# Kernel tuning notes

Hardware: AMD Instinct MI355X
Metric: run time of the kernel (lower is better)

Reference implementation:

```python
import jax, jax.numpy as jnp
import numpy as np

B, D, H, W = 4, 64, 64, 64
S = 64          # number of attention segments
N = 8192        # query pixels
K = 4           # n_refs
HID = 256
D9 = D * 9      # feat_unfold 3x3
IN_DIM = D9 + 2 + 2  # +rel_coord +rel_cell


def setup_inputs() -> dict:
    key = jax.random.key(0)
    ks = jax.random.split(key, 10)
    feat = jax.random.normal(ks[0], (B, D, H, W), jnp.float32)
    attn_sftmx = jax.nn.softmax(jax.random.normal(ks[1], (B, H * W, S), jnp.float32), axis=2)
    coord = jax.random.uniform(ks[2], (B, N, 2), jnp.float32) * 2.0 - 1.0  # [-1,1]
    cell = jnp.full((B, N, 2), 2.0 / 256.0, jnp.float32)  # HR cell size for 256x256 output
    def lin(k, fi, fo):
        return jax.random.normal(k, (fi, fo), jnp.float32) / np.sqrt(fi).astype(np.float32)
    w0 = lin(ks[3], IN_DIM, HID); b0 = jnp.zeros((HID,), jnp.float32)
    w1 = lin(ks[4], HID, HID);    b1 = jnp.zeros((HID,), jnp.float32)
    w2 = lin(ks[5], HID, HID);    b2 = jnp.zeros((HID,), jnp.float32)
    w3 = lin(ks[6], HID, HID);    b3 = jnp.zeros((HID,), jnp.float32)
    w4 = lin(ks[7], HID, 3);      b4 = jnp.zeros((3,), jnp.float32)
    return dict(feat=feat, attn_sftmx=attn_sftmx, coord=coord, cell=cell,
                w0=w0, b0=b0, w1=w1, b1=b1, w2=w2, b2=b2, w3=w3, b3=b3, w4=w4, b4=b4)


def _imnet(x, w0, b0, w1, b1, w2, b2, w3, b3, w4, b4):
    h = jax.nn.relu(x @ w0 + b0)
    h = jax.nn.relu(h @ w1 + b1)
    h = jax.nn.relu(h @ w2 + b2)
    h = jax.nn.relu(h @ w3 + b3)
    return h @ w4 + b4


def reference(feat, attn_sftmx, coord, cell, w0, b0, w1, b1, w2, b2, w3, b3, w4, b4):
    Bn, Dc, h, w = feat.shape
    Nq = coord.shape[1]
    hw = h * w
    # ---- feat_unfold: F.unfold(feat, 3, padding=1) -> (B, D*9, h, w), channel order c*9 + ki*3 + kj
    pad = jnp.pad(feat, ((0, 0), (0, 0), (1, 1), (1, 1)))
    patches = jnp.stack([pad[:, :, ki:ki + h, kj:kj + w]
                         for ki in range(3) for kj in range(3)], axis=2)  # (B,D,9,h,w)
    d9 = Dc * 9
    feat_rows = patches.reshape(Bn, d9, h, w).transpose(0, 2, 3, 1).reshape(Bn, hw, d9)  # (B,hw,D9)
    scale_hw = jnp.array([h, w], jnp.float32)
    rel_cell = cell * scale_hw  # (B,N,2)

    # ================= attention ensemble =================
    pc = (coord + 1.0) / 2.0 * scale_hw
    pc = jnp.clip(pc.astype(jnp.int32), 0, hw - 1)
    pc1d = pc[..., 0] * h + pc[..., 1]  # (B,N)
    segm_idx_whole = jnp.argmax(attn_sftmx, axis=2)  # (B,hw)
    segm_idx = jnp.take_along_axis(segm_idx_whole, pc1d, axis=1)  # (B,N)
    attn_t = attn_sftmx.transpose(0, 2, 1)  # (B,S,hw)
    prob_map = jnp.take_along_axis(attn_t, segm_idx[:, :, None], axis=1)  # (B,N,hw)
    ref_probs, ref_coords = jax.lax.top_k(prob_map, K)  # (B,N,K)
    # Faithful to original: ref_coords (values in [0,hw)) index the FLATTENED (B*hw, D9)
    # feature table, i.e. all batches gather batch-0 rows (source-code behavior).
    ref_feats = feat_rows.reshape(Bn * hw, d9)[ref_coords]  # (B,N,K,D9)
    rrc = ref_coords - pc1d[..., None]  # (B,N,K) int
    rel0 = jnp.floor_divide(rrc, h).astype(jnp.float32) / h
    rel1 = jnp.mod(rrc, h).astype(jnp.float32) / w
    rel = jnp.stack([rel0, rel1], axis=-1)  # (B,N,K,2)
    rc_b = jnp.broadcast_to(rel_cell[:, :, None, :], (Bn, Nq, K, 2))
    inp_attn = jnp.concatenate([ref_feats, rel, rc_b], axis=-1)  # (B,N,K,IN)
    pred_attn = _imnet(inp_attn.reshape(-1, inp_attn.shape[-1]),
                       w0, b0, w1, b1, w2, b2, w3, b3, w4, b4).reshape(Bn, Nq, K, -1)
    wprob = ref_probs / jnp.sum(ref_probs, axis=-1, keepdims=True)
    ret_attn = jnp.sum(pred_attn * wprob[..., None], axis=2)  # (B,N,3)

    # ================= local ensemble =================
    rx, ry = 1.0 / h, 1.0 / w  # 2/h/2, 2/w/2
    eps = 1e-6
    offs = jnp.array([[-1., -1.], [-1., 1.], [1., -1.], [1., 1.]], jnp.float32) \
           * jnp.array([rx, ry], jnp.float32) + eps  # (4,2)
    c = jnp.clip(coord[None] + offs[:, None, None, :], -1 + 1e-6, 1 - 1e-6)  # (4,B,N,2)
    # grid_sample nearest, align_corners=False (grid flipped -> c[...,0] is height)
    iy = jnp.clip(jnp.rint(((c[..., 0] + 1.0) * h - 1.0) / 2.0), 0, h - 1).astype(jnp.int32)
    ix = jnp.clip(jnp.rint(((c[..., 1] + 1.0) * w - 1.0) / 2.0), 0, w - 1).astype(jnp.int32)
    flat = iy * w + ix  # (4,B,N)
    bidx = jnp.arange(Bn)[None, :, None]
    q_feat = feat_rows[bidx, flat]  # (4,B,N,D9)
    qc0 = -1.0 + (2.0 * iy.astype(jnp.float32) + 1.0) / h  # make_coord centers
    qc1 = -1.0 + (2.0 * ix.astype(jnp.float32) + 1.0) / w
    rel_coord = jnp.stack([(coord[None, ..., 0] - qc0) * h,
                           (coord[None, ..., 1] - qc1) * w], axis=-1)  # (4,B,N,2)
    rc_l = jnp.broadcast_to(rel_cell[None], (4, Bn, Nq, 2))
    inp_loc = jnp.concatenate([q_feat, rel_coord, rc_l], axis=-1)  # (4,B,N,IN)
    pred_loc = _imnet(inp_loc.reshape(-1, inp_loc.shape[-1]),
                      w0, b0, w1, b1, w2, b2, w3, b3, w4, b4).reshape(4, Bn, Nq, -1)
    area = jnp.abs(rel_coord[..., 0] * rel_coord[..., 1]) + 1e-9  # (4,B,N)
    tot = jnp.sum(area, axis=0)
    wts = area[::-1] / tot[None]  # area swap 0<->3, 1<->2 == reverse
    ret_local = jnp.sum(pred_loc * wts[..., None], axis=0)  # (B,N,3)

    total = float(K + 4)
    return ret_attn * (K / total) + ret_local * (4.0 / total)
```

## Files before the change

kernel.cpp:

```cpp
#include <hip/hip_runtime.h>
#include <hip/hip_bf16.h>
#include <math.h>
#include <stdint.h>

#define B_ 4
#define D_ 64
#define H_ 64
#define W_ 64
#define S_ 64
#define N_ 8192
#define K_ 4
#define HID_ 256
#define HW_ 4096
#define NQ_ (B_*N_)
#define ROWS_ (NQ_*8)

typedef _Float16 h8   __attribute__((ext_vector_type(8)));
typedef _Float16 h4   __attribute__((ext_vector_type(4)));
typedef float    f32x4 __attribute__((ext_vector_type(4)));

__global__ void fused_prep_kernel(const float* __restrict__ feat,
                                  const float* __restrict__ attn,
                                  const float* __restrict__ w0,
                                  const float* __restrict__ w1,
                                  const float* __restrict__ w2,
                                  const float* __restrict__ w3,
                                  const float* __restrict__ w4,
                                  _Float16* __restrict__ featT,
                                  _Float16* __restrict__ w0F,
                                  _Float16* __restrict__ wF123,
                                  float* __restrict__ w4T,
                                  float* __restrict__ w0tail,
                                  int* __restrict__ segm,
                                  float* __restrict__ pv,
                                  int* __restrict__ pi)
{
  __shared__ float t[64][65];
  int blk = blockIdx.x;
  int tid = threadIdx.x;

  if (blk < 256) {
    int b = blk >> 6, y = blk & 63;
    for (int p = 0; p < 16; ++p) {
      int c = p * 4 + (tid >> 6), x = tid & 63;
      t[c][x] = feat[(((size_t)b * 64 + c) << 12) + (y << 6) + x];
    }
    __syncthreads();
    for (int p = 0; p < 16; ++p) {
      int x = p * 4 + (tid >> 6), c = tid & 63;
      featT[((((size_t)b * 64 + y) * 64 + x) << 6) + c] = (_Float16)t[c][x];
    }
    return;
  }
  blk -= 256;
  if (blk < 1351) {
    int i = blk * 256 + tid;
    if (i < 147456) {
      int g = i / 36864, rem = i - g * 36864;
      int ks = rem >> 11, rem2 = rem & 2047;
      int cb = rem2 >> 9, e = rem2 & 511;
      int lane = e >> 3, j = e & 7;
      int n = g * 64 + cb * 16 + (lane & 15);
      int k = ks * 32 + (lane >> 4) * 8 + j;
      int kk = k >> 6, cc = k & 63;
      w0F[i] = (_Float16)w0[(cc * 9 + kk) * 256 + n];
      return;
    }
    i -= 147456;
    if (i < 196608) {
      int l = i >> 16, rem = i & 65535;
      int g = rem >> 14, rem2 = rem & 16383;
      int ks = rem2 >> 11, rem3 = rem2 & 2047;
      int cb = rem3 >> 9, e = rem3 & 511;
      int lane = e >> 3, j = e & 7;
      int n = g * 64 + cb * 16 + (lane & 15);
      int k = ks * 32 + (lane >> 4) * 8 + j;
      const float* w = (l == 0) ? w1 : (l == 1) ? w2 : w3;
      wF123[i] = (_Float16)w[k * 256 + n];
      return;
    }
    i -= 196608;
    if (i < 768) { int j = i / 256, c = i - j * 256; w4T[i] = w4[c * 3 + j]; return; }
    i -= 768;
    if (i < 1024) { int j = i >> 8, n = i & 255; w0tail[i] = w0[(576 + j) * 256 + n]; }
    return;
  }
  blk -= 1351;
  {
    int b = blk >> 6, chunk = blk & 63;
    int j0 = chunk * 64;
    for (int idx = tid; idx < 4096; idx += 256) {
      int r = idx >> 6, c = idx & 63;
      t[r][c] = attn[((size_t)(b * 4096 + j0 + r)) * 64 + c];
    }
    __syncthreads();
    if (tid >= 64 && tid < 128) {
      int r = tid - 64;
      float best = t[r][0]; int bi = 0;
      for (int s = 1; s < 64; ++s) { float v = t[r][s]; if (v > best) { best = v; bi = s; } }
      segm[b * 4096 + j0 + r] = bi;
    } else if (tid < 64) {
      int s = tid;
      float tv[4] = { -INFINITY, -INFINITY, -INFINITY, -INFINITY };
      int   ti[4] = { 0x7fffffff, 0x7fffffff, 0x7fffffff, 0x7fffffff };
      for (int r = 0; r < 64; ++r) {
        float v = t[r][s];
        if (v > tv[3]) {
          tv[3] = v; ti[3] = j0 + r;
          #pragma unroll
          for (int x = 3; x > 0; --x) {
            if (tv[x] > tv[x-1] || (tv[x] == tv[x-1] && ti[x] < ti[x-1])) {
              float fv = tv[x]; tv[x] = tv[x-1]; tv[x-1] = fv;
              int   fi = ti[x]; ti[x] = ti[x-1]; ti[x-1] = fi;
            }
          }
        }
      }
      size_t base = (((size_t)(b * 64 + s)) * 64 + chunk) * 4;
      #pragma unroll
      for (int k = 0; k < 4; ++k) { pv[base + k] = tv[k]; pi[base + k] = ti[k]; }
    }
  }
}

__global__ void meta_kernel(const float* __restrict__ coord, const float* __restrict__ cell,
                            const int* __restrict__ segm,
                            const float* __restrict__ pv, const int* __restrict__ pi,
                            int* __restrict__ msrc, float4* __restrict__ mt,
                            float* __restrict__ mwgt)
{
  __shared__ int   refcL[64][4];
  __shared__ float wprobL[64][4];
  int tid = threadIdx.x;
  int bb = blockIdx.x >> 5;
  if (tid < 64) {
    int s = tid;
    float tv[4] = { -INFINITY, -INFINITY, -INFINITY, -INFINITY };
    int   ti[4] = { 0x7fffffff, 0x7fffffff, 0x7fffffff, 0x7fffffff };
    size_t base = ((size_t)(bb * 64 + s)) * 256;
    for (int c = 0; c < 256; ++c) {
      float v = pv[base + c]; int ix = pi[base + c];
      if (v > tv[3] || (v == tv[3] && ix < ti[3])) {
        tv[3] = v; ti[3] = ix;
        #pragma unroll
        for (int x = 3; x > 0; --x) {
          if (tv[x] > tv[x-1] || (tv[x] == tv[x-1] && ti[x] < ti[x-1])) {
            float fv = tv[x]; tv[x] = tv[x-1]; tv[x-1] = fv;
            int   fi = ti[x]; ti[x] = ti[x-1]; ti[x-1] = fi;
          }
        }
      }
    }
    float ssum = tv[0] + tv[1] + tv[2] + tv[3];
    #pragma unroll
    for (int k = 0; k < 4; ++k) { refcL[s][k] = ti[k]; wprobL[s][k] = tv[k] / ssum; }
  }
  __syncthreads();

  int q = blockIdx.x * 256 + tid;
  int b = q >> 13;
  float c0 = coord[2*q], c1 = coord[2*q + 1];
  float rc0 = cell[2*q] * 64.0f, rc1 = cell[2*q + 1] * 64.0f;

  float pf0 = (c0 + 1.0f) / 2.0f * 64.0f;
  float pf1 = (c1 + 1.0f) / 2.0f * 64.0f;
  int pc0 = (int)pf0, pc1 = (int)pf1;
  pc0 = min(max(pc0, 0), 4095); pc1 = min(max(pc1, 0), 4095);
  int pc1d = pc0 * 64 + pc1;
  int sg = segm[b * 4096 + min(pc1d, 4095)];
  #pragma unroll
  for (int k = 0; k < 4; ++k) {
    int rc = refcL[sg][k];
    int rrc = rc - pc1d;
    float rel0 = (float)(rrc >> 6) * 0.015625f;
    float rel1 = (float)(rrc & 63) * 0.015625f;
    int r = q * 8 + k;
    msrc[r] = rc;
    mt[r] = make_float4(rel0, rel1, rc0, rc1);
    mwgt[r] = 0.5f * wprobL[sg][k];
  }

  const float sg0[4] = { -1.f, -1.f, 1.f, 1.f };
  const float sg1[4] = { -1.f,  1.f, -1.f, 1.f };
  float area[4], rr0[4], rr1[4]; int srcs[4];
  #pragma unroll
  for (int tt = 0; tt < 4; ++tt) {
    float o0 = sg0[tt] * 0.015625f + 1e-6f;
    float o1 = sg1[tt] * 0.015625f + 1e-6f;
    float cc0 = fminf(fmaxf(c0 + o0, -1.0f + 1e-6f), 1.0f - 1e-6f);
    float cc1 = fminf(fmaxf(c1 + o1, -1.0f + 1e-6f), 1.0f - 1e-6f);
    float vy = ((cc0 + 1.0f) * 64.0f - 1.0f) / 2.0f;
    float vx = ((cc1 + 1.0f) * 64.0f - 1.0f) / 2.0f;
    float fy = fminf(fmaxf(rintf(vy), 0.0f), 63.0f);
    float fx = fminf(fmaxf(rintf(vx), 0.0f), 63.0f);
    int iy = (int)fy, ix = (int)fx;
    srcs[tt] = b * 4096 + iy * 64 + ix;
    float qc0 = -1.0f + (2.0f * (float)iy + 1.0f) / 64.0f;
    float qc1 = -1.0f + (2.0f * (float)ix + 1.0f) / 64.0f;
    float r0 = (c0 - qc0) * 64.0f;
    float r1 = (c1 - qc1) * 64.0f;
    rr0[tt] = r0; rr1[tt] = r1;
    area[tt] = fabsf(r0 * r1) + 1e-9f;
  }
  float tot = area[0] + area[1] + area[2] + area[3];
  #pragma unroll
  for (int tt = 0; tt < 4; ++tt) {
    int r = q * 8 + 4 + tt;
    msrc[r] = srcs[tt];
    mt[r] = make_float4(rr0[tt], rr1[tt], rc0, rc1);
    mwgt[r] = 0.5f * area[3 - tt] / tot;
  }
}

__launch_bounds__(256, 2)
__global__ void p0_kernel(const _Float16* __restrict__ featT,
                          const _Float16* __restrict__ w0F,
                          _Float16* __restrict__ P0h)
{
  int blk = blockIdx.x;
  int b = blk >> 7, y = (blk >> 1) & 63, hr = blk & 1;
  int tid = threadIdx.x;
  int wave = tid >> 6, lane = tid & 63, quad = lane >> 4, l16 = lane & 15;

  f32x4 acc[2][4];
  #pragma unroll
  for (int i = 0; i < 2; i++)
    #pragma unroll
    for (int j = 0; j < 4; j++) { f32x4 z = {0.f,0.f,0.f,0.f}; acc[i][j] = z; }
  h8 zero8 = {0,0,0,0,0,0,0,0};

  #pragma unroll
  for (int ks = 0; ks < 18; ++ks) {
    int k0 = ks * 32 + quad * 8;
    int kk = k0 >> 6, cc = k0 & 63;
    int di = kk / 3 - 1, dj = kk - (kk / 3) * 3 - 1;
    int yy = y + di;
    h8 afr[2];
    #pragma unroll
    for (int rb = 0; rb < 2; rb++) {
      int xx = hr * 32 + rb * 16 + l16 + dj;
      if ((unsigned)yy < 64u && (unsigned)xx < 64u)
        afr[rb] = *(const h8*)(featT + ((((size_t)b * 64 + yy) * 64 + xx) << 6) + cc);
      else
        afr[rb] = zero8;
    }
    h8 bfr[4];
    #pragma unroll
    for (int cb = 0; cb < 4; cb++)
      bfr[cb] = *(const h8*)(w0F + ((((size_t)wave * 18 + ks) * 4 + cb) << 9) + lane * 8);
    #pragma unroll
    for (int rb = 0; rb < 2; rb++)
      #pragma unroll
      for (int cb = 0; cb < 4; cb++)
        acc[rb][cb] = __builtin_amdgcn_mfma_f32_16x16x32_f16(afr[rb], bfr[cb], acc[rb][cb], 0, 0, 0);
  }
  int pixbase = b * 4096 + y * 64 + hr * 32;
  #pragma unroll
  for (int rb = 0; rb < 2; rb++)
    #pragma unroll
    for (int cb = 0; cb < 4; cb++)
      #pragma unroll
      for (int i = 0; i < 4; i++) {
        int m = rb * 16 + quad * 4 + i;
        int n = wave * 64 + cb * 16 + l16;
        P0h[((size_t)(pixbase + m) << 8) + n] = (_Float16)acc[rb][cb][i];
      }
}

__launch_bounds__(256, 2)
__global__ void trunk_kernel(const _Float16* __restrict__ P0h,
                             const int* __restrict__ msrc,
                             const float4* __restrict__ mt,
                             const float* __restrict__ mwgt,
                             const float* __restrict__ w0tail,
                             const float* __restrict__ b0,
                             const _Float16* __restrict__ wF123,
                             const float* __restrict__ b1,
                             const float* __restrict__ b2,
                             const float* __restrict__ b3,
                             const float* __restrict__ w4T,
                             const float* __restrict__ b4,
                             float* __restrict__ out)
{
  __shared__ _Float16 hS[128][264];
  __shared__ float mwL[128];
  __shared__ float swL[16];
  __shared__ float partB[16][3][4];

  int tid = threadIdx.x;
  int rowbase = blockIdx.x * 128;
  int wv = tid >> 6;

  if (tid < 128) mwL[tid] = mwgt[rowbase + tid];

  {
    int cg = tid & 63;
    float4 wt0 = ((const float4*)w0tail)[cg];
    float4 wt1 = ((const float4*)w0tail)[64 + cg];
    float4 wt2 = ((const float4*)w0tail)[128 + cg];
    float4 wt3 = ((const float4*)w0tail)[192 + cg];
    float4 bb  = ((const float4*)b0)[cg];
    #pragma unroll 1
    for (int g = 0; g < 4; ++g) {
      int srcs[8]; float4 ts[8];
      #pragma unroll
      for (int i = 0; i < 8; ++i) {
        int r = rowbase + g * 32 + i * 4 + wv;
        srcs[i] = msrc[r];
        ts[i] = mt[r];
      }
      #pragma unroll
      for (int i = 0; i < 8; ++i) {
        int rr = g * 32 + i * 4 + wv;
        float4 t = ts[i];
        h4 pvv = *(const h4*)(P0h + ((size_t)srcs[i] << 8) + cg * 4);
        h4 v;
        v[0] = (_Float16)fmaxf((float)pvv[0] + t.x*wt0.x + t.y*wt1.x + t.z*wt2.x + t.w*wt3.x + bb.x, 0.0f);
        v[1] = (_Float16)fmaxf((float)pvv[1] + t.x*wt0.y + t.y*wt1.y + t.z*wt2.y + t.w*wt3.y + bb.y, 0.0f);
        v[2] = (_Float16)fmaxf((float)pvv[2] + t.x*wt0.z + t.y*wt1.z + t.z*wt2.z + t.w*wt3.z + bb.z, 0.0f);
        v[3] = (_Float16)fmaxf((float)pvv[3] + t.x*wt0.w + t.y*wt1.w + t.z*wt2.w + t.w*wt3.w + bb.w, 0.0f);
        *(h4*)(&hS[rr][cg * 4]) = v;
      }
    }
  }
  __syncthreads();

  int wave = tid >> 6, lane = tid & 63, quad = lane >> 4, l16 = lane & 15;

  #pragma unroll 1
  for (int l = 0; l < 3; ++l) {
    const _Float16* wL = wF123 + (((size_t)l * 4 + wave) << 14);
    const float* bia = (l == 0) ? b1 : (l == 1) ? b2 : b3;
    f32x4 acc[8][4];
    #pragma unroll
    for (int i = 0; i < 8; i++)
      #pragma unroll
      for (int j = 0; j < 4; j++) { f32x4 z = {0.f,0.f,0.f,0.f}; acc[i][j] = z; }

    h8 bP[2][4];
    #pragma unroll
    for (int cb = 0; cb < 4; cb++) {
      bP[0][cb] = *(const h8*)(wL + (((size_t)0 * 4 + cb) << 9) + lane * 8);
      bP[1][cb] = *(const h8*)(wL + (((size_t)1 * 4 + cb) << 9) + lane * 8);
    }

    #pragma unroll
    for (int ks = 0; ks < 8; ++ks) {
      int cur = ks & 1;
      int k0 = ks * 32 + quad * 8;
      h8 afr[8];
      #pragma unroll
      for (int rb = 0; rb < 8; rb++)
        afr[rb] = *(const h8*)(&hS[rb * 16 + l16][k0]);
      #pragma unroll
      for (int rb = 0; rb < 8; rb++)
        #pragma unroll
        for (int cb = 0; cb < 4; cb++)
          acc[rb][cb] = __builtin_amdgcn_mfma_f32_16x16x32_f16(afr[rb], bP[cur][cb], acc[rb][cb], 0, 0, 0);
      if (ks + 2 < 8) {
        #pragma unroll
        for (int cb = 0; cb < 4; cb++)
          bP[cur][cb] = *(const h8*)(wL + (((size_t)(ks + 2) * 4 + cb) << 9) + lane * 8);
      }
    }
    __syncthreads();
    #pragma unroll
    for (int rb = 0; rb < 8; rb++)
      #pragma unroll
      for (int cb = 0; cb < 4; cb++) {
        int n = wave * 64 + cb * 16 + l16;
        float bv = bia[n];
        #pragma unroll
        for (int i = 0; i < 4; i++) {
          int m = rb * 16 + quad * 4 + i;
          hS[m][n] = (_Float16)fmaxf(acc[rb][cb][i] + bv, 0.0f);
        }
      }
    __syncthreads();
  }

  {
    if (tid < 16) {
      float sw = 0.0f;
      #pragma unroll
      for (int j = 0; j < 8; ++j) sw += mwL[tid * 8 + j];
      swL[tid] = sw;
    }
    int c = tid;
    float accq[16];
    #pragma unroll
    for (int u = 0; u < 16; ++u) accq[u] = 0.0f;
    #pragma unroll
    for (int row = 0; row < 128; ++row) {
      float w = mwL[row];
      accq[row >> 3] += w * (float)hS[row][c];
    }
    __syncthreads();
    float* hsF = (float*)&hS[0][0];
    #pragma unroll
    for (int q = 0; q < 16; ++q) hsF[q * 256 + c] = accq[q];
  }
  __syncthreads();
  if (tid < 192) {
    int q = tid / 12, r = tid % 12, j = r >> 2, part = r & 3;
    const float* hsF = (const float*)&hS[0][0];
    const float* hp = hsF + q * 256 + part * 64;
    const float* wp = w4T + j * 256 + part * 64;
    int u0 = tid & 63;
    float s = 0.0f;
    #pragma unroll
    for (int u = 0; u < 64; ++u) {
      int uu = (u0 + u) & 63;
      s += hp[uu] * wp[uu];
    }
    partB[q][j][part] = s;
  }
  __syncthreads();
  if (tid < 48) {
    int q = tid / 3, j = tid % 3;
    float o = partB[q][j][0] + partB[q][j][1] + partB[q][j][2] + partB[q][j][3]
            + b4[j] * swL[q];
    out[(size_t)(blockIdx.x * 16 + q) * 3 + j] = o;
  }
}

extern "C" void kernel_launch(void* const* d_in, const int* in_sizes, int n_in,
                              void* d_out, int out_size, void* d_ws, size_t ws_size,
                              hipStream_t stream)
{
  const float* feat  = (const float*)d_in[0];
  const float* attn  = (const float*)d_in[1];
  const float* coord = (const float*)d_in[2];
  const float* cell  = (const float*)d_in[3];
  const float* w0 = (const float*)d_in[4];
  const float* b0 = (const float*)d_in[5];
  const float* w1 = (const float*)d_in[6];
  const float* b1 = (const float*)d_in[7];
  const float* w2 = (const float*)d_in[8];
  const float* b2 = (const float*)d_in[9];
  const float* w3 = (const float*)d_in[10];
  const float* b3 = (const float*)d_in[11];
  const float* w4 = (const float*)d_in[12];
  const float* b4 = (const float*)d_in[13];
  float* out = (float*)d_out;

  char* ws = (char*)d_ws;
  size_t off = 0;
  auto alloc = [&](size_t bytes) -> char* {
    char* p = ws + off;
    off += (bytes + 255) & ~(size_t)255;
    return p;
  };
  _Float16* featT = (_Float16*)alloc((size_t)B_ * H_ * W_ * D_ * 2);
  _Float16* w0F   = (_Float16*)alloc((size_t)147456 * 2);
  _Float16* wF123 = (_Float16*)alloc((size_t)196608 * 2);
  float*  w4T   = (float*)alloc((size_t)3 * 256 * 4);
  float*  w0tl  = (float*)alloc((size_t)4 * 256 * 4);
  int*    segm  = (int*)alloc((size_t)B_ * HW_ * 4);
  float*  pv    = (float*)alloc((size_t)B_ * S_ * 64 * 4 * 4);
  int*    pi    = (int*)alloc((size_t)B_ * S_ * 64 * 4 * 4);
  _Float16* P0h = (_Float16*)alloc((size_t)B_ * HW_ * 256 * 2);
  int*    msrc  = (int*)alloc((size_t)ROWS_ * 4);
  float4* mtb   = (float4*)alloc((size_t)ROWS_ * 16);
  float*  mwgt  = (float*)alloc((size_t)ROWS_ * 4);
  (void)in_sizes; (void)n_in; (void)out_size; (void)ws_size;

  fused_prep_kernel<<<1863, 256, 0, stream>>>(feat, attn, w0, w1, w2, w3, w4,
                                              featT, w0F, wF123, w4T, w0tl,
                                              segm, pv, pi);
  meta_kernel<<<128, 256, 0, stream>>>(coord, cell, segm, pv, pi, msrc, mtb, mwgt);
  p0_kernel<<<512, 256, 0, stream>>>(featT, w0F, P0h);
  trunk_kernel<<<2048, 256, 0, stream>>>(P0h, msrc, mtb, mwgt, w0tl, b0, wF123,
                                         b1, b2, b3, w4T, b4, out);
}
```

Before: 291.4 us.

## Move per-segment top-4 merge into extra p0 block, vectorize trunk reduction

The segment top-4 merge, which meta_kernel used to recompute redundantly in every block, now runs once in a single extra block (block 512) of p0_kernel and writes refc and wprob to global memory. meta_kernel becomes a purely per-query kernel that reads those arrays. This removes duplicated serial work, at the cost of one block doing a long serial merge inside p0. The trunk epilogue's weighted row reduction is also rewritten so each thread reads 16 consecutive channels of its query's 8 rows with vector loads and stores. The rotated index in the final dot product is dropped, which may bring back LDS bank conflicts.

```diff
diff --git a/kernel.cpp b/kernel.cpp
--- a/kernel.cpp
+++ b/kernel.cpp
@@ -123,21 +123,19 @@
   }
 }
 
-__global__ void meta_kernel(const float* __restrict__ coord, const float* __restrict__ cell,
-                            const int* __restrict__ segm,
-                            const float* __restrict__ pv, const int* __restrict__ pi,
-                            int* __restrict__ msrc, float4* __restrict__ mt,
-                            float* __restrict__ mwgt)
+__launch_bounds__(256, 2)
+__global__ void p0_kernel(const _Float16* __restrict__ featT,
+                          const _Float16* __restrict__ w0F,
+                          const float* __restrict__ pv, const int* __restrict__ pi,
+                          _Float16* __restrict__ P0h,
+                          int* __restrict__ refc, float* __restrict__ wprob)
 {
-  __shared__ int   refcL[64][4];
-  __shared__ float wprobL[64][4];
+  int blk = blockIdx.x;
   int tid = threadIdx.x;
-  int bb = blockIdx.x >> 5;
-  if (tid < 64) {
-    int s = tid;
+  if (blk == 512) {
     float tv[4] = { -INFINITY, -INFINITY, -INFINITY, -INFINITY };
     int   ti[4] = { 0x7fffffff, 0x7fffffff, 0x7fffffff, 0x7fffffff };
-    size_t base = ((size_t)(bb * 64 + s)) * 256;
+    size_t base = (size_t)tid * 256;
     for (int c = 0; c < 256; ++c) {
       float v = pv[base + c]; int ix = pi[base + c];
       if (v > tv[3] || (v == tv[3] && ix < ti[3])) {
@@ -153,11 +151,66 @@
     }
     float ssum = tv[0] + tv[1] + tv[2] + tv[3];
     #pragma unroll
-    for (int k = 0; k < 4; ++k) { refcL[s][k] = ti[k]; wprobL[s][k] = tv[k] / ssum; }
-  }
-  __syncthreads();
-
-  int q = blockIdx.x * 256 + tid;
+    for (int k = 0; k < 4; ++k) { refc[tid*4 + k] = ti[k]; wprob[tid*4 + k] = tv[k] / ssum; }
+    return;
+  }
+
+  int b = blk >> 7, y = (blk >> 1) & 63, hr = blk & 1;
+  int wave = tid >> 6, lane = tid & 63, quad = lane >> 4, l16 = lane & 15;
+
+  f32x4 acc[2][4];
+  #pragma unroll
+  for (int i = 0; i < 2; i++)
+    #pragma unroll
+    for (int j = 0; j < 4; j++) { f32x4 z = {0.f,0.f,0.f,0.f}; acc[i][j] = z; }
+  h8 zero8 = {0,0,0,0,0,0,0,0};
+
+  #pragma unroll
+  for (int ks = 0; ks < 18; ++ks) {
+    int k0 = ks * 32 + quad * 8;
+    int kk = k0 >> 6, cc = k0 & 63;
+    int di = kk / 3 - 1, dj = kk - (kk / 3) * 3 - 1;
+    int yy = y + di;
+    h8 afr[2];
+    #pragma unroll
+    for (int rb = 0; rb < 2; rb++) {
+      int xx = hr * 32 + rb * 16 + l16 + dj;
+      if ((unsigned)yy < 64u && (unsigned)xx < 64u)
+        afr[rb] = *(const h8*)(featT + ((((size_t)b * 64 + yy) * 64 + xx) << 6) + cc);
+      else
+        afr[rb] = zero8;
+    }
+    h8 bfr[4];
+    #pragma unroll
+    for (int cb = 0; cb < 4; cb++)
+      bfr[cb] = *(const h8*)(w0F + ((((size_t)wave * 18 + ks) * 4 + cb) << 9) + lane * 8);
+    #pragma unroll
+    for (int rb = 0; rb < 2; rb++)
+      #pragma unroll
+      for (int cb = 0; cb < 4; cb++)
+        acc[rb][cb] = __builtin_amdgcn_mfma_f32_16x16x32_f16(afr[rb], bfr[cb], acc[rb][cb], 0, 0, 0);
+  }
+  int pixbase = b * 4096 + y * 64 + hr * 32;
+  #pragma unroll
+  for (int rb = 0; rb < 2; rb++)
+    #pragma unroll
+    for (int cb = 0; cb < 4; cb++)
+      #pragma unroll
+      for (int i = 0; i < 4; i++) {
+        int m = rb * 16 + quad * 4 + i;
+        int n = wave * 64 + cb * 16 + l16;
+        P0h[((size_t)(pixbase + m) << 8) + n] = (_Float16)acc[rb][cb][i];
+      }
+}
+
+__global__ void meta_kernel(const float* __restrict__ coord, const float* __restrict__ cell,
+                            const int* __restrict__ segm, const int* __restrict__ refc,
+                            const float* __restrict__ wprob,
+                            int* __restrict__ msrc, float4* __restrict__ mt,
+                            float* __restrict__ mwgt)
+{
+  int q = blockIdx.x * 256 + threadIdx.x;
+  if (q >= NQ_) return;
   int b = q >> 13;
   float c0 = coord[2*q], c1 = coord[2*q + 1];
   float rc0 = cell[2*q] * 64.0f, rc1 = cell[2*q + 1] * 64.0f;
@@ -168,25 +221,26 @@
   pc0 = min(max(pc0, 0), 4095); pc1 = min(max(pc1, 0), 4095);
   int pc1d = pc0 * 64 + pc1;
   int sg = segm[b * 4096 + min(pc1d, 4095)];
+  int base = (b * 64 + sg) * 4;
   #pragma unroll
   for (int k = 0; k < 4; ++k) {
-    int rc = refcL[sg][k];
+    int rc = refc[base + k];
     int rrc = rc - pc1d;
     float rel0 = (float)(rrc >> 6) * 0.015625f;
     float rel1 = (float)(rrc & 63) * 0.015625f;
     int r = q * 8 + k;
     msrc[r] = rc;
     mt[r] = make_float4(rel0, rel1, rc0, rc1);
-    mwgt[r] = 0.5f * wprobL[sg][k];
+    mwgt[r] = 0.5f * wprob[base + k];
   }
 
   const float sg0[4] = { -1.f, -1.f, 1.f, 1.f };
   const float sg1[4] = { -1.f,  1.f, -1.f, 1.f };
   float area[4], rr0[4], rr1[4]; int srcs[4];
   #pragma unroll
-  for (int tt = 0; tt < 4; ++tt) {
-    float o0 = sg0[tt] * 0.015625f + 1e-6f;
-    float o1 = sg1[tt] * 0.015625f + 1e-6f;
+  for (int t = 0; t < 4; ++t) {
+    float o0 = sg0[t] * 0.015625f + 1e-6f;
+    float o1 = sg1[t] * 0.015625f + 1e-6f;
     float cc0 = fminf(fmaxf(c0 + o0, -1.0f + 1e-6f), 1.0f - 1e-6f);
     float cc1 = fminf(fmaxf(c1 + o1, -1.0f + 1e-6f), 1.0f - 1e-6f);
     float vy = ((cc0 + 1.0f) * 64.0f - 1.0f) / 2.0f;
@@ -194,77 +248,22 @@
     float fy = fminf(fmaxf(rintf(vy), 0.0f), 63.0f);
     float fx = fminf(fmaxf(rintf(vx), 0.0f), 63.0f);
     int iy = (int)fy, ix = (int)fx;
-    srcs[tt] = b * 4096 + iy * 64 + ix;
+    srcs[t] = b * 4096 + iy * 64 + ix;
     float qc0 = -1.0f + (2.0f * (float)iy + 1.0f) / 64.0f;
     float qc1 = -1.0f + (2.0f * (float)ix + 1.0f) / 64.0f;
     float r0 = (c0 - qc0) * 64.0f;
     float r1 = (c1 - qc1) * 64.0f;
-    rr0[tt] = r0; rr1[tt] = r1;
-    area[tt] = fabsf(r0 * r1) + 1e-9f;
+    rr0[t] = r0; rr1[t] = r1;
+    area[t] = fabsf(r0 * r1) + 1e-9f;
   }
   float tot = area[0] + area[1] + area[2] + area[3];
   #pragma unroll
-  for (int tt = 0; tt < 4; ++tt) {
-    int r = q * 8 + 4 + tt;
-    msrc[r] = srcs[tt];
-    mt[r] = make_float4(rr0[tt], rr1[tt], rc0, rc1);
-    mwgt[r] = 0.5f * area[3 - tt] / tot;
-  }
-}
-
-__launch_bounds__(256, 2)
-__global__ void p0_kernel(const _Float16* __restrict__ featT,
-                          const _Float16* __restrict__ w0F,
-                          _Float16* __restrict__ P0h)
-{
-  int blk = blockIdx.x;
-  int b = blk >> 7, y = (blk >> 1) & 63, hr = blk & 1;
-  int tid = threadIdx.x;
-  int wave = tid >> 6, lane = tid & 63, quad = lane >> 4, l16 = lane & 15;
-
-  f32x4 acc[2][4];
-  #pragma unroll
-  for (int i = 0; i < 2; i++)
-    #pragma unroll
-    for (int j = 0; j < 4; j++) { f32x4 z = {0.f,0.f,0.f,0.f}; acc[i][j] = z; }
-  h8 zero8 = {0,0,0,0,0,0,0,0};
-
-  #pragma unroll
-  for (int ks = 0; ks < 18; ++ks) {
-    int k0 = ks * 32 + quad * 8;
-    int kk = k0 >> 6, cc = k0 & 63;
-    int di = kk / 3 - 1, dj = kk - (kk / 3) * 3 - 1;
-    int yy = y + di;
-    h8 afr[2];
-    #pragma unroll
-    for (int rb = 0; rb < 2; rb++) {
-      int xx = hr * 32 + rb * 16 + l16 + dj;
-      if ((unsigned)yy < 64u && (unsigned)xx < 64u)
-        afr[rb] = *(const h8*)(featT + ((((size_t)b * 64 + yy) * 64 + xx) << 6) + cc);
-      else
-        afr[rb] = zero8;
-    }
-    h8 bfr[4];
-    #pragma unroll
-    for (int cb = 0; cb < 4; cb++)
-      bfr[cb] = *(const h8*)(w0F + ((((size_t)wave * 18 + ks) * 4 + cb) << 9) + lane * 8);
-    #pragma unroll
-    for (int rb = 0; rb < 2; rb++)
-      #pragma unroll
-      for (int cb = 0; cb < 4; cb++)
-        acc[rb][cb] = __builtin_amdgcn_mfma_f32_16x16x32_f16(afr[rb], bfr[cb], acc[rb][cb], 0, 0, 0);
-  }
-  int pixbase = b * 4096 + y * 64 + hr * 32;
-  #pragma unroll
-  for (int rb = 0; rb < 2; rb++)
-    #pragma unroll
-    for (int cb = 0; cb < 4; cb++)
-      #pragma unroll
-      for (int i = 0; i < 4; i++) {
-        int m = rb * 16 + quad * 4 + i;
-        int n = wave * 64 + cb * 16 + l16;
-        P0h[((size_t)(pixbase + m) << 8) + n] = (_Float16)acc[rb][cb][i];
-      }
+  for (int t = 0; t < 4; ++t) {
+    int r = q * 8 + 4 + t;
+    msrc[r] = srcs[t];
+    mt[r] = make_float4(rr0[t], rr1[t], rc0, rc1);
+    mwgt[r] = 0.5f * area[3 - t] / tot;
+  }
 }
 
 __launch_bounds__(256, 2)
@@ -380,25 +379,31 @@
   }
 
   {
-    if (tid < 16) {
-      float sw = 0.0f;
-      #pragma unroll
-      for (int j = 0; j < 8; ++j) sw += mwL[tid * 8 + j];
-      swL[tid] = sw;
-    }
-    int c = tid;
+    int q = tid >> 4, cpart = tid & 15;
     float accq[16];
     #pragma unroll
     for (int u = 0; u < 16; ++u) accq[u] = 0.0f;
-    #pragma unroll
-    for (int row = 0; row < 128; ++row) {
+    float sw = 0.0f;
+    #pragma unroll
+    for (int j = 0; j < 8; ++j) {
+      int row = q * 8 + j;
       float w = mwL[row];
-      accq[row >> 3] += w * (float)hS[row][c];
+      sw += w;
+      h8 a = *(const h8*)(&hS[row][cpart * 16]);
+      h8 bq = *(const h8*)(&hS[row][cpart * 16 + 8]);
+      #pragma unroll
+      for (int u = 0; u < 8; ++u) {
+        accq[u]     += w * (float)a[u];
+        accq[8 + u] += w * (float)bq[u];
+      }
     }
     __syncthreads();
     float* hsF = (float*)&hS[0][0];
     #pragma unroll
-    for (int q = 0; q < 16; ++q) hsF[q * 256 + c] = accq[q];
+    for (int u = 0; u < 16; u += 4)
+      *(f32x4*)(hsF + q * 256 + cpart * 16 + u) =
+        f32x4{accq[u], accq[u+1], accq[u+2], accq[u+3]};
+    if (cpart == 0) swL[q] = sw;
   }
   __syncthreads();
   if (tid < 192) {
@@ -406,13 +411,9 @@
     const float* hsF = (const float*)&hS[0][0];
     const float* hp = hsF + q * 256 + part * 64;
     const float* wp = w4T + j * 256 + part * 64;
-    int u0 = tid & 63;
     float s = 0.0f;
     #pragma unroll
-    for (int u = 0; u < 64; ++u) {
-      int uu = (u0 + u) & 63;
-      s += hp[uu] * wp[uu];
-    }
+    for (int u = 0; u < 64; ++u) s += hp[u] * wp[u];
     partB[q][j][part] = s;
   }
   __syncthreads();
@@ -459,6 +460,8 @@
   int*    segm  = (int*)alloc((size_t)B_ * HW_ * 4);
   float*  pv    = (float*)alloc((size_t)B_ * S_ * 64 * 4 * 4);
   int*    pi    = (int*)alloc((size_t)B_ * S_ * 64 * 4 * 4);
+  int*    refc  = (int*)alloc((size_t)B_ * S_ * K_ * 4);
+  float*  wprob = (float*)alloc((size_t)B_ * S_ * K_ * 4);
   _Float16* P0h = (_Float16*)alloc((size_t)B_ * HW_ * 256 * 2);
   int*    msrc  = (int*)alloc((size_t)ROWS_ * 4);
   float4* mtb   = (float4*)alloc((size_t)ROWS_ * 16);
@@ -468,8 +471,8 @@
   fused_prep_kernel<<<1863, 256, 0, stream>>>(feat, attn, w0, w1, w2, w3, w4,
                                               featT, w0F, wF123, w4T, w0tl,
                                               segm, pv, pi);
-  meta_kernel<<<128, 256, 0, stream>>>(coord, cell, segm, pv, pi, msrc, mtb, mwgt);
-  p0_kernel<<<512, 256, 0, stream>>>(featT, w0F, P0h);
+  p0_kernel<<<513, 256, 0, stream>>>(featT, w0F, pv, pi, P0h, refc, wprob);
+  meta_kernel<<<128, 256, 0, stream>>>(coord, cell, segm, refc, wprob, msrc, mtb, mwgt);
   trunk_kernel<<<2048, 256, 0, stream>>>(P0h, msrc, mtb, mwgt, w0tl, b0, wF123,
                                          b1, b2, b3, w4T, b4, out);
 }
```

New measurement: 304.6 us. 1.05x slower.
